# Optimization experiments

Measured on AMD Instinct MI355X. Metric: run time of the kernel, lower is better.

The kernel has to match this reference:

```python
import jax, jax.numpy as jnp
import numpy as np

N = 716      # number of nodes (hard-coded in module)
T = 12       # time_len (hard-coded)
C = 10       # in_channels (hard-coded)
B = 64       # batch size
DEG = 8 + (np.arange(N) % 17)   # variable per-node neighbor counts (ragged)
E = int(DEG.sum())              # 11441 total neighbor slots


def setup_inputs() -> dict:
    key = jax.random.key(0)
    ks = jax.random.split(key, 8)
    seg_ids = jnp.asarray(np.repeat(np.arange(N), DEG), dtype=jnp.int32)  # [E]
    return {
        "neighbor_vals": jax.random.normal(ks[0], (B, T, E), jnp.float32),
        "W_flat": jax.random.normal(ks[1], (C, E), jnp.float32) * 0.1,  # concat of per-node Linear weights
        "bias": jax.random.normal(ks[2], (N, C), jnp.float32) * 0.1,    # per-node Linear bias
        "W1": jax.random.normal(ks[3], (T,), jnp.float32),
        "W2": jax.random.normal(ks[4], (C, T), jnp.float32),
        "W3": jax.random.normal(ks[5], (C,), jnp.float32),
        "bs": jax.random.normal(ks[6], (1, N, N), jnp.float32),
        "Vs": jax.random.normal(ks[7], (N, N), jnp.float32),
        "seg_ids": seg_ids,
    }


def reference(neighbor_vals, W_flat, bias, W1, W2, W3, bs, Vs, seg_ids):
    # --- ragged per-node Linear (was a Python triple loop in torch) ---
    # emb[b,t,n,c] = sum_{e in node n} vals[b,t,e] * W_flat[c,e] + bias[n,c]
    vals_e = jnp.transpose(neighbor_vals, (2, 0, 1))              # [E,B,T]
    contrib = vals_e[..., None] * W_flat.T[:, None, None, :]      # [E,B,T,C]
    emb = jax.ops.segment_sum(contrib, seg_ids, num_segments=N)   # [N,B,T,C]
    x = jnp.transpose(emb, (1, 0, 3, 2)) + bias[None, :, :, None] # [B,N,C,T]

    # --- spatial attention chain ---
    lhs = jnp.einsum('bnct,t->bnc', x, W1) @ W2                   # [B,N,T]
    rhs = jnp.einsum('c,bnct->bnt', W3, x)                        # [B,N,T] (rhs.T applied in einsum below)
    product = jnp.einsum('bnt,bmt->bnm', lhs, rhs)                # [B,N,N]
    S = jnp.einsum('nm,bmk->bnk', Vs, jax.nn.sigmoid(product + bs))
    return jax.nn.softmax(S, axis=1)
```

## Files before the change

### kernel.cpp

```cpp
#include <hip/hip_runtime.h>
#include <cstdint>

using u16 = unsigned short;
using f16 = _Float16;

static constexpr int N = 716;
static constexpr int T = 12;
static constexpr int C = 10;
static constexpr int B = 64;
static constexpr int E = 11441;

static constexpr int KP = 768;
static constexpr int BK = 64;
static constexpr int NSTEP = KP / BK;

typedef __attribute__((ext_vector_type(8))) f16 f16x8;
typedef __attribute__((ext_vector_type(4))) float f32x4;

__device__ __forceinline__ int node_off(int n) {
    int q = n / 17, r = n % 17;
    return 8 * n + 136 * q + (r * (r - 1)) / 2;
}

typedef const __attribute__((address_space(1))) unsigned int* gp1_t;
typedef __attribute__((address_space(3))) unsigned int* lp3_t;
__device__ __forceinline__ void gload16(const void* g, void* l) {
    __builtin_amdgcn_global_load_lds((gp1_t)g, (lp3_t)l, 16, 0, 0);
}

__device__ __forceinline__ float wsum(float p) {
#pragma unroll
    for (int o = 1; o < 64; o <<= 1) p += __shfl_xor(p, o);
    return p;
}

static constexpr int KB_PLANES = (N * KP) / 256;
static constexpr int KB_BST    = (N * N + 255) / 256;
static constexpr int KB_RS     = N;

__global__ void __launch_bounds__(256) k_static(const float* __restrict__ Vs,
                                                const float* __restrict__ bs,
                                                f16* __restrict__ AH, f16* __restrict__ AL,
                                                float* __restrict__ bsT, float* __restrict__ rs) {
    int blk = blockIdx.x;
    if (blk < KB_PLANES) {
        int idx = blk * 256 + threadIdx.x;
        int n = idx / KP, ic = idx - n * KP;
        float v = (ic < N) ? Vs[(size_t)n * N + ic] : 0.f;
        f16 hi = (f16)v;
        AH[idx] = hi;
        AL[idx] = (f16)(v - (float)hi);
    } else if (blk < KB_PLANES + KB_BST) {
        int idx = (blk - KB_PLANES) * 256 + threadIdx.x;
        if (idx < N * N) {
            int j = idx / N, i = idx - j * N;
            bsT[(size_t)j * N + i] = bs[(size_t)i * N + j];
        }
    } else {
        int n = blk - (KB_PLANES + KB_BST);
        float s = 0.f;
        for (int i = threadIdx.x; i < N; i += 256) s += Vs[(size_t)n * N + i];
#pragma unroll
        for (int o = 32; o >= 1; o >>= 1) s += __shfl_xor(s, o);
        __shared__ float red[4];
        if ((threadIdx.x & 63) == 0) red[threadIdx.x >> 6] = s;
        __syncthreads();
        if (threadIdx.x == 0) rs[n] = red[0] + red[1] + red[2] + red[3];
    }
}

__global__ void __launch_bounds__(256) k_fused_ln(const float* __restrict__ vals,
                                                  const float* __restrict__ W_flat,
                                                  const float* __restrict__ bias,
                                                  const float* __restrict__ W1,
                                                  const float* __restrict__ W2,
                                                  const float* __restrict__ W3,
                                                  float* __restrict__ rhs,
                                                  float* __restrict__ lhs) {
    int wid = blockIdx.x * 4 + (threadIdx.x >> 6);
    int lane = threadIdx.x & 63;
    int b = wid / N, n = wid - b * N;
    int off = node_off(n);
    int deg = 8 + (n % 17);
    bool act = lane < deg;

    float w1[T];
    float S1 = 0.f;
#pragma unroll
    for (int t = 0; t < T; ++t) { w1[t] = W1[t]; S1 += w1[t]; }

    float wv = 0.f;
#pragma unroll
    for (int c = 0; c < C; ++c)
        wv += W3[c] * (act ? W_flat[(size_t)c * E + off + lane] : 0.f);

    float bbv = 0.f;
#pragma unroll
    for (int c = 0; c < C; ++c) bbv += W3[c] * bias[n * C + c];

    float u = 0.f;
    float rloc[T];
#pragma unroll
    for (int t = 0; t < T; ++t) {
        float v = act ? vals[((size_t)b * T + t) * E + off + lane] : 0.f;
        u = fmaf(v, w1[t], u);
        rloc[t] = wsum(v * wv) + bbv;
    }

    float lh[T];
#pragma unroll
    for (int t = 0; t < T; ++t) lh[t] = 0.f;
#pragma unroll
    for (int c = 0; c < C; ++c) {
        float p = act ? u * W_flat[(size_t)c * E + off + lane] : 0.f;
        float ac = wsum(p) + S1 * bias[n * C + c];
#pragma unroll
        for (int t = 0; t < T; ++t) lh[t] = fmaf(ac, W2[c * T + t], lh[t]);
    }

    float outv_r = 0.f, outv_l = 0.f;
#pragma unroll
    for (int t = 0; t < T; ++t)
        if (lane == t) { outv_r = rloc[t]; outv_l = lh[t]; }
    if (lane < T) {
        size_t base = ((size_t)b * N + n) * T + lane;
        rhs[base] = outv_r;
        lhs[base] = outv_l;
    }
}

__global__ void __launch_bounds__(256) k_prod2(const float* __restrict__ lhs,
                                               const float* __restrict__ rhs,
                                               const float* __restrict__ bsT,
                                               f16* __restrict__ T16) {
    __shared__ float rl[16][12];
    int tid = threadIdx.x;
    int b = blockIdx.z;
    int j0 = blockIdx.y * 16;
    int i = blockIdx.x * 256 + tid;
    if (tid < 192) {
        int jj = tid / 12, t = tid - jj * 12;
        int j = j0 + jj;
        rl[jj][t] = (j < N) ? rhs[((size_t)b * N + j) * T + t] : 0.f;
    }
    __syncthreads();
    float l[12];
    bool live = (i < N);
    if (live) {
        const float4* lp = (const float4*)(lhs + ((size_t)b * N + i) * T);
        float4 a0 = lp[0], a1 = lp[1], a2 = lp[2];
        l[0] = a0.x; l[1] = a0.y; l[2] = a0.z; l[3] = a0.w;
        l[4] = a1.x; l[5] = a1.y; l[6] = a1.z; l[7] = a1.w;
        l[8] = a2.x; l[9] = a2.y; l[10] = a2.z; l[11] = a2.w;
    }
#pragma unroll
    for (int jj = 0; jj < 16; ++jj) {
        int j = j0 + jj;
        if (j >= N) break;
        size_t dst = ((size_t)b * N + j) * KP + i;
        if (live) {
            float s = bsT[(size_t)j * N + i];
#pragma unroll
            for (int t = 0; t < T; ++t) s = fmaf(l[t], rl[jj][t], s);
            float v = 1.f / (1.f + __expf(-s)) - 0.5f;
            T16[dst] = (f16)v;
        } else {
            T16[dst] = (f16)0.f;
        }
    }
}

__global__ void __launch_bounds__(256, 3)
k_mfma(const f16* __restrict__ AH, const f16* __restrict__ AL,
       const f16* __restrict__ Bp, const float* __restrict__ rs,
       float* __restrict__ S, float* __restrict__ pmax, float* __restrict__ psum) {
    __shared__ f16 lds[3][128 * BK];
    __shared__ float smx[2][2][64];
    __shared__ float ssm[2][2][64];
    const int tid = threadIdx.x;
    const int bz = blockIdx.z;
    const int nt = blockIdx.y, jt = blockIdx.x;
    const int n0 = nt * 128, j0 = jt * 128;
    const int lane = tid & 63;
    const int wid = tid >> 6;
    const int wr = wid >> 1, wc = wid & 1;
    const int r = lane & 15, h = lane >> 4;

    const f16* srcB = Bp + (size_t)bz * N * KP;

    const int cb_sw = ((tid & 7) * 16) ^ (((tid >> 3) & 7) * 16);
    const int row_base = tid >> 3;

    f32x4 acc[4][4] = {};

    for (int step = 0; step < NSTEP; ++step) {
        const int mb = step * (BK * 2);
#pragma unroll
        for (int p = 0; p < 3; ++p) {
            const int rbase = (p < 2) ? n0 : j0;
            const f16* src = (p == 0) ? AH : (p == 1) ? AL : srcB;
#pragma unroll
            for (int q = 0; q < 4; ++q) {
                int lrow = q * 32 + row_base;
                int grow = rbase + lrow;
                if (grow > N - 1) grow = N - 1;
                const char* g = (const char*)src + (size_t)grow * (KP * 2) + mb + cb_sw;
                gload16(g, (char*)&lds[p][0] + q * 4096 + tid * 16);
            }
        }
        __syncthreads();
#pragma unroll
        for (int kk = 0; kk < 2; ++kk) {
            f16x8 aHf[4], aLf[4], bf[4];
#pragma unroll
            for (int f = 0; f < 4; ++f) {
                int arow = wr * 64 + f * 16 + r;
                int aidx = arow * BK + ((kk * 32 + h * 8) ^ ((arow & 7) * 8));
                aHf[f] = *(const f16x8*)&lds[0][aidx];
                aLf[f] = *(const f16x8*)&lds[1][aidx];
                int brow = wc * 64 + f * 16 + r;
                int bidx = brow * BK + ((kk * 32 + h * 8) ^ ((brow & 7) * 8));
                bf[f] = *(const f16x8*)&lds[2][bidx];
            }
#pragma unroll
            for (int fi = 0; fi < 4; ++fi)
#pragma unroll
                for (int fj = 0; fj < 4; ++fj) {
                    acc[fi][fj] = __builtin_amdgcn_mfma_f32_16x16x32_f16(aHf[fi], bf[fj], acc[fi][fj], 0, 0, 0);
                    acc[fi][fj] = __builtin_amdgcn_mfma_f32_16x16x32_f16(aLf[fi], bf[fj], acc[fi][fj], 0, 0, 0);
                }
        }
        __syncthreads();
    }

    float rsv[4][4];
#pragma unroll
    for (int fi = 0; fi < 4; ++fi)
#pragma unroll
        for (int qq = 0; qq < 4; ++qq) {
            int rg = n0 + wr * 64 + fi * 16 + h * 4 + qq;
            rsv[fi][qq] = (rg < N) ? 0.5f * rs[rg] : 0.f;
        }
#pragma unroll
    for (int fi = 0; fi < 4; ++fi)
#pragma unroll
        for (int fj = 0; fj < 4; ++fj)
#pragma unroll
            for (int qq = 0; qq < 4; ++qq) acc[fi][fj][qq] += rsv[fi][qq];

    float* Sb = S + (size_t)bz * N * N;
#pragma unroll
    for (int fi = 0; fi < 4; ++fi) {
        int rg = n0 + wr * 64 + fi * 16 + h * 4;
#pragma unroll
        for (int fj = 0; fj < 4; ++fj) {
            int cg = j0 + wc * 64 + fj * 16 + r;
            if (cg < N) {
#pragma unroll
                for (int qq = 0; qq < 4; ++qq)
                    if (rg + qq < N) Sb[(size_t)(rg + qq) * N + cg] = acc[fi][fj][qq];
            }
        }
    }

#pragma unroll
    for (int fj = 0; fj < 4; ++fj) {
        float m = -3.0e38f;
#pragma unroll
        for (int fi = 0; fi < 4; ++fi)
#pragma unroll
            for (int qq = 0; qq < 4; ++qq) {
                int rg = n0 + wr * 64 + fi * 16 + h * 4 + qq;
                float v = (rg < N) ? acc[fi][fj][qq] : -3.0e38f;
                m = fmaxf(m, v);
            }
        m = fmaxf(m, __shfl_xor(m, 16));
        m = fmaxf(m, __shfl_xor(m, 32));
        float s = 0.f;
#pragma unroll
        for (int fi = 0; fi < 4; ++fi)
#pragma unroll
            for (int qq = 0; qq < 4; ++qq) {
                int rg = n0 + wr * 64 + fi * 16 + h * 4 + qq;
                if (rg < N) s += __expf(acc[fi][fj][qq] - m);
            }
        s += __shfl_xor(s, 16);
        s += __shfl_xor(s, 32);
        if (lane < 16) {
            smx[wr][wc][fj * 16 + lane] = m;
            ssm[wr][wc][fj * 16 + lane] = s;
        }
    }
    __syncthreads();
    if (tid < 128) {
        int wcc = tid >> 6, c = tid & 63;
        float m0 = smx[0][wcc][c], m1 = smx[1][wcc][c];
        float m = fmaxf(m0, m1);
        float s = ssm[0][wcc][c] * __expf(m0 - m) + ssm[1][wcc][c] * __expf(m1 - m);
        int j = j0 + wcc * 64 + c;
        size_t o = ((size_t)bz * 6 + nt) * 768 + j;
        pmax[o] = m;
        psum[o] = s;
    }
}

__global__ void __launch_bounds__(256) k_norm3(float* __restrict__ S,
                                               const float* __restrict__ pmax,
                                               const float* __restrict__ psum) {
    __shared__ float smaxL[64];
    __shared__ float sinvL[64];
    int jt = blockIdx.x, b = blockIdx.y;
    int j0 = jt * 64;
    int tid = threadIdx.x;
    if (tid < 64) {
        int j = j0 + tid;
        float m = -3.0e38f, s = 0.f;
        if (j < N) {
#pragma unroll
            for (int c = 0; c < 6; ++c) m = fmaxf(m, pmax[((size_t)b * 6 + c) * 768 + j]);
#pragma unroll
            for (int c = 0; c < 6; ++c)
                s += psum[((size_t)b * 6 + c) * 768 + j] * __expf(pmax[((size_t)b * 6 + c) * 768 + j] - m);
        } else {
            s = 1.f;
        }
        smaxL[tid] = m;
        sinvL[tid] = 1.f / s;
    }
    __syncthreads();

    int rowo = tid >> 4;
    int q = tid & 15;
    int jj = q * 4;
    if (j0 + jj >= N) return;
    float m0 = smaxL[jj], m1 = smaxL[jj + 1], m2 = smaxL[jj + 2], m3 = smaxL[jj + 3];
    float r0 = sinvL[jj], r1 = sinvL[jj + 1], r2 = sinvL[jj + 2], r3 = sinvL[jj + 3];
    float* Sb = S + (size_t)b * N * N + j0 + jj;
    for (int r = rowo; r < N; r += 16) {
        float4 v = *(float4*)(Sb + (size_t)r * N);
        v.x = __expf(v.x - m0) * r0;
        v.y = __expf(v.y - m1) * r1;
        v.z = __expf(v.z - m2) * r2;
        v.w = __expf(v.w - m3) * r3;
        *(float4*)(Sb + (size_t)r * N) = v;
    }
}

extern "C" void kernel_launch(void* const* d_in, const int* in_sizes, int n_in,
                              void* d_out, int out_size, void* d_ws, size_t ws_size,
                              hipStream_t stream) {
    const float* vals   = (const float*)d_in[0];
    const float* W_flat = (const float*)d_in[1];
    const float* bias   = (const float*)d_in[2];
    const float* W1     = (const float*)d_in[3];
    const float* W2     = (const float*)d_in[4];
    const float* W3     = (const float*)d_in[5];
    const float* bs     = (const float*)d_in[6];
    const float* Vs     = (const float*)d_in[7];
    float* out = (float*)d_out;

    float* f = (float*)d_ws;
    f16* sigT = (f16*)f;   f += (size_t)B * N * KP / 2;
    f16* AHp  = (f16*)f;   f += (size_t)N * KP / 2;
    f16* ALp  = (f16*)f;   f += (size_t)N * KP / 2;
    float* rhs  = f;  f += (size_t)B * N * T;
    float* lhs  = f;  f += (size_t)B * N * T;
    float* bsT  = f;  f += (size_t)N * N;
    float* rsw  = f;  f += 720;
    float* pmax = f;  f += (size_t)B * 6 * 768;
    float* psum = f;  f += (size_t)B * 6 * 768;

    k_static<<<KB_PLANES + KB_BST + KB_RS, 256, 0, stream>>>(Vs, bs, AHp, ALp, bsT, rsw);

    k_fused_ln<<<(B * N) / 4, 256, 0, stream>>>(vals, W_flat, bias, W1, W2, W3, rhs, lhs);

    dim3 gp(3, (N + 15) / 16, B);
    k_prod2<<<gp, 256, 0, stream>>>(lhs, rhs, bsT, sigT);

    dim3 gg((N + 127) / 128, (N + 127) / 128, B);
    k_mfma<<<gg, 256, 0, stream>>>(AHp, ALp, sigT, rsw, out, pmax, psum);

    k_norm3<<<dim3(12, B), 256, 0, stream>>>(out, pmax, psum);
}
```

Before: 478.3 us.

## Split MFMA launch into batch chunks and flatten softmax normalization

Launches the MFMA GEMM as four chunked launches of 16 batches each instead of one big grid. The final column-softmax normalization is split into a small combine kernel that merges the per-tile max and sum partials, followed by a fully flat elementwise normalize kernel with one thread per float4. The flat kernel is meant to expose far more parallelism and better coalescing than the old 12x64-block kernel, which looped over rows. The cost is extra kernel launches, and chunking the GEMM may help cache locality or may add launch gaps.

```diff
diff --git a/kernel.cpp b/kernel.cpp
--- a/kernel.cpp
+++ b/kernel.cpp
@@ -13,6 +13,7 @@
 static constexpr int KP = 768;
 static constexpr int BK = 64;
 static constexpr int NSTEP = KP / BK;
+static constexpr int MCH = 16;
 
 typedef __attribute__((ext_vector_type(8))) f16 f16x8;
 typedef __attribute__((ext_vector_type(4))) float f32x4;
@@ -173,12 +174,13 @@
 __global__ void __launch_bounds__(256, 3)
 k_mfma(const f16* __restrict__ AH, const f16* __restrict__ AL,
        const f16* __restrict__ Bp, const float* __restrict__ rs,
-       float* __restrict__ S, float* __restrict__ pmax, float* __restrict__ psum) {
+       float* __restrict__ S, float* __restrict__ pmax, float* __restrict__ psum,
+       int b0) {
     __shared__ f16 lds[3][128 * BK];
     __shared__ float smx[2][2][64];
     __shared__ float ssm[2][2][64];
     const int tid = threadIdx.x;
-    const int bz = blockIdx.z;
+    const int bz = b0 + blockIdx.z;
     const int nt = blockIdx.y, jt = blockIdx.x;
     const int n0 = nt * 128, j0 = jt * 128;
     const int lane = tid & 63;
@@ -304,46 +306,40 @@
     }
 }
 
-__global__ void __launch_bounds__(256) k_norm3(float* __restrict__ S,
-                                               const float* __restrict__ pmax,
-                                               const float* __restrict__ psum) {
-    __shared__ float smaxL[64];
-    __shared__ float sinvL[64];
-    int jt = blockIdx.x, b = blockIdx.y;
-    int j0 = jt * 64;
-    int tid = threadIdx.x;
-    if (tid < 64) {
-        int j = j0 + tid;
-        float m = -3.0e38f, s = 0.f;
-        if (j < N) {
-#pragma unroll
-            for (int c = 0; c < 6; ++c) m = fmaxf(m, pmax[((size_t)b * 6 + c) * 768 + j]);
-#pragma unroll
-            for (int c = 0; c < 6; ++c)
-                s += psum[((size_t)b * 6 + c) * 768 + j] * __expf(pmax[((size_t)b * 6 + c) * 768 + j] - m);
-        } else {
-            s = 1.f;
-        }
-        smaxL[tid] = m;
-        sinvL[tid] = 1.f / s;
-    }
-    __syncthreads();
-
-    int rowo = tid >> 4;
-    int q = tid & 15;
-    int jj = q * 4;
-    if (j0 + jj >= N) return;
-    float m0 = smaxL[jj], m1 = smaxL[jj + 1], m2 = smaxL[jj + 2], m3 = smaxL[jj + 3];
-    float r0 = sinvL[jj], r1 = sinvL[jj + 1], r2 = sinvL[jj + 2], r3 = sinvL[jj + 3];
-    float* Sb = S + (size_t)b * N * N + j0 + jj;
-    for (int r = rowo; r < N; r += 16) {
-        float4 v = *(float4*)(Sb + (size_t)r * N);
-        v.x = __expf(v.x - m0) * r0;
-        v.y = __expf(v.y - m1) * r1;
-        v.z = __expf(v.z - m2) * r2;
-        v.w = __expf(v.w - m3) * r3;
-        *(float4*)(Sb + (size_t)r * N) = v;
-    }
+__global__ void k_comb(const float* __restrict__ pmax, const float* __restrict__ psum,
+                       float* __restrict__ smax, float* __restrict__ sinv) {
+    int i = blockIdx.x * 256 + threadIdx.x;
+    if (i >= B * N) return;
+    int b = i / N, j = i - b * N;
+    float m = -3.0e38f;
+#pragma unroll
+    for (int c = 0; c < 6; ++c) m = fmaxf(m, pmax[((size_t)b * 6 + c) * 768 + j]);
+    float s = 0.f;
+#pragma unroll
+    for (int c = 0; c < 6; ++c)
+        s += psum[((size_t)b * 6 + c) * 768 + j] * __expf(pmax[((size_t)b * 6 + c) * 768 + j] - m);
+    smax[(size_t)b * 720 + j] = m;
+    sinv[(size_t)b * 720 + j] = 1.f / s;
+}
+
+__global__ void k_norm2(float* __restrict__ S, const float* __restrict__ smax,
+                        const float* __restrict__ sinv) {
+    size_t idx = (size_t)blockIdx.x * 256 + threadIdx.x;
+    if (idx >= (size_t)B * N * (N / 4)) return;
+    int jq = (int)(idx % (N / 4));
+    size_t bn = idx / (N / 4);
+    int n = (int)(bn % N);
+    int b = (int)(bn / N);
+    size_t base = ((size_t)b * N + n) * N + (size_t)jq * 4;
+    int j = jq * 4;
+    float4 v = *(float4*)(S + base);
+    float4 mm = *(const float4*)(smax + (size_t)b * 720 + j);
+    float4 rr = *(const float4*)(sinv + (size_t)b * 720 + j);
+    v.x = __expf(v.x - mm.x) * rr.x;
+    v.y = __expf(v.y - mm.y) * rr.y;
+    v.z = __expf(v.z - mm.z) * rr.z;
+    v.w = __expf(v.w - mm.w) * rr.w;
+    *(float4*)(S + base) = v;
 }
 
 extern "C" void kernel_launch(void* const* d_in, const int* in_sizes, int n_in,
@@ -369,6 +365,8 @@
     float* rsw  = f;  f += 720;
     float* pmax = f;  f += (size_t)B * 6 * 768;
     float* psum = f;  f += (size_t)B * 6 * 768;
+    float* smax = f;  f += (size_t)B * 720;
+    float* sinv = f;  f += (size_t)B * 720;
 
     k_static<<<KB_PLANES + KB_BST + KB_RS, 256, 0, stream>>>(Vs, bs, AHp, ALp, bsT, rsw);
 
@@ -377,8 +375,13 @@
     dim3 gp(3, (N + 15) / 16, B);
     k_prod2<<<gp, 256, 0, stream>>>(lhs, rhs, bsT, sigT);
 
-    dim3 gg((N + 127) / 128, (N + 127) / 128, B);
-    k_mfma<<<gg, 256, 0, stream>>>(AHp, ALp, sigT, rsw, out, pmax, psum);
-
-    k_norm3<<<dim3(12, B), 256, 0, stream>>>(out, pmax, psum);
-}
+    for (int c = 0; c < B / MCH; ++c) {
+        dim3 gg((N + 127) / 128, (N + 127) / 128, MCH);
+        k_mfma<<<gg, 256, 0, stream>>>(AHp, ALp, sigT, rsw, out, pmax, psum, c * MCH);
+    }
+
+    k_comb<<<(B * N + 255) / 256, 256, 0, stream>>>(pmax, psum, smax, sinv);
+
+    size_t nv = (size_t)B * N * (N / 4);
+    k_norm2<<<(int)((nv + 255) / 256), 256, 0, stream>>>(out, smax, sinv);
+}
```

After: 500.9 us. 1.05x slower.
